# Optimization experiments

Hardware: AMD Instinct MI355X
Metric: run time of the kernel (lower is better)

Reference implementation:

```python
import jax, jax.numpy as jnp
import numpy as np

D_MODEL = 1024
D_STATE = 16
D_CONV = 4
EXPAND = 2
D_INNER = EXPAND * D_MODEL
BATCH = 2
SEQ = 4096


def setup_inputs() -> dict:
    key = jax.random.key(0)
    ks = jax.random.split(key, 8)
    def w(k, shape, fan_in):
        return jax.random.normal(k, shape, jnp.float32) * (fan_in ** -0.5)
    x = jax.random.normal(ks[0], (BATCH, SEQ, D_MODEL), jnp.float32)
    in_proj_w = w(ks[1], (2 * D_INNER, D_MODEL), D_MODEL)
    conv_w = w(ks[2], (D_INNER, 1, D_CONV), D_CONV)          # depthwise conv kernel (OIH, groups=D_INNER)
    conv_b = jnp.zeros((D_INNER,), jnp.float32)
    x_proj_w = w(ks[3], (1 + 2 * D_STATE, D_INNER), D_INNER)
    dt_proj_w = w(ks[4], (D_INNER, 1), D_STATE)               # Linear(1 -> d_inner), see notes
    dt_proj_b = jnp.zeros((D_INNER,), jnp.float32)
    A_log = jnp.log(jnp.tile(jnp.arange(1, D_STATE + 1, dtype=jnp.float32)[None, :], (D_INNER, 1)))
    D = jnp.ones((D_INNER,), jnp.float32)
    out_proj_w = w(ks[5], (D_MODEL, D_INNER), D_INNER)
    return dict(x=x, in_proj_w=in_proj_w, conv_w=conv_w, conv_b=conv_b,
                x_proj_w=x_proj_w, dt_proj_w=dt_proj_w, dt_proj_b=dt_proj_b,
                A_log=A_log, D=D, out_proj_w=out_proj_w)


def _selective_scan(xs, delta, Bm, Cm, A, D):
    # xs, delta: [B, L, d_inner]; Bm, Cm: [B, L, d_state]; A: [d_inner, d_state]
    def step(h, inp):
        x_t, d_t, b_t, c_t = inp                      # [B,di],[B,di],[B,n],[B,n]
        dA = jnp.exp(d_t[..., None] * A)              # [B, di, n]
        h = dA * h + (d_t * x_t)[..., None] * b_t[:, None, :]
        y = jnp.einsum('bdn,bn->bd', h, c_t) + D * x_t
        return h, y
    h0 = jnp.zeros((xs.shape[0], xs.shape[2], A.shape[1]), xs.dtype)
    seq = (jnp.swapaxes(xs, 0, 1), jnp.swapaxes(delta, 0, 1),
           jnp.swapaxes(Bm, 0, 1), jnp.swapaxes(Cm, 0, 1))
    _, ys = jax.lax.scan(step, h0, seq)               # ys: [L, B, di]
    return jnp.swapaxes(ys, 0, 1)


def _mamba(x, in_proj_w, conv_w, conv_b, x_proj_w, dt_proj_w, dt_proj_b, A_log, D, out_proj_w):
    xz = x @ in_proj_w.T                               # [B, L, 2*di]
    xc, z = jnp.split(xz, 2, axis=-1)
    # causal depthwise conv (pad left d_conv-1, truncate to seq_len)
    u = jnp.swapaxes(xc, 1, 2)                         # [B, di, L]
    u = jax.lax.conv_general_dilated(
        u, conv_w, window_strides=(1,), padding=[(D_CONV - 1, 0)],
        feature_group_count=D_INNER, dimension_numbers=('NCH', 'OIH', 'NCH'))
    u = u + conv_b[None, :, None]
    xs = jax.nn.silu(jnp.swapaxes(u, 1, 2))            # [B, L, di]
    dbc = xs @ x_proj_w.T                              # [B, L, 1+2n]
    delta_raw = dbc[..., :1]
    Bm = dbc[..., 1:1 + D_STATE]
    Cm = dbc[..., 1 + D_STATE:]
    delta = jax.nn.softplus(delta_raw @ dt_proj_w.T + dt_proj_b)   # [B, L, di]
    A = -jnp.exp(A_log)
    y = _selective_scan(xs, delta, Bm, Cm, A, D)
    return (y * jax.nn.silu(z)) @ out_proj_w.T


def reference(x, in_proj_w, conv_w, conv_b, x_proj_w, dt_proj_w, dt_proj_b, A_log, D, out_proj_w):
    return _mamba(x, in_proj_w, conv_w, conv_b, x_proj_w, dt_proj_w, dt_proj_b, A_log, D, out_proj_w)
```

## Files before the change

### kernel.cpp

```cpp
#include <hip/hip_runtime.h>
#include <hip/hip_bf16.h>
#include <stdint.h>

typedef __bf16 bf16x8 __attribute__((ext_vector_type(8)));
typedef float  f32x4  __attribute__((ext_vector_type(4)));
typedef unsigned short u16x8 __attribute__((ext_vector_type(8)));

#define TC 64
#define NC 64

__device__ __forceinline__ unsigned short f2bf(float f) {
  unsigned u = __builtin_bit_cast(unsigned, f);
  unsigned r = (u + 0x7fffu + ((u >> 16) & 1u)) >> 16;
  return (unsigned short)r;
}
__device__ __forceinline__ float bf2f(unsigned short s) {
  unsigned u = ((unsigned)s) << 16;
  return __builtin_bit_cast(float, u);
}

__device__ __forceinline__ void gload_lds16(const void* g, void* l) {
  __builtin_amdgcn_global_load_lds(
      (const __attribute__((address_space(1))) unsigned int*)(g),
      (__attribute__((address_space(3))) unsigned int*)(l),
      16, 0, 0);
}

__device__ __forceinline__ void rpowers(float r, float* rp) {
  float r2 = r * r, r4 = r2 * r2, r8 = r4 * r4;
  rp[0] = r;        rp[1] = r2;       rp[2] = r2 * r;   rp[3] = r4;
  rp[4] = r4 * r;   rp[5] = r4 * r2;  rp[6] = rp[5] * r; rp[7] = r8;
  rp[8] = r8 * r;   rp[9] = r8 * r2;  rp[10] = rp[9] * r; rp[11] = r8 * r4;
  rp[12] = rp[11] * r; rp[13] = rp[11] * r2; rp[14] = rp[13] * r; rp[15] = r8 * r8;
}

__global__ __launch_bounds__(256) void cast_bf16_k(const float4* __restrict__ in,
                                                   ushort4* __restrict__ out, int n4) {
  int i = blockIdx.x * 256 + threadIdx.x;
  int stride = gridDim.x * 256;
  for (; i < n4; i += stride) {
    float4 v = in[i];
    ushort4 o;
    o.x = f2bf(v.x); o.y = f2bf(v.y); o.z = f2bf(v.z); o.w = f2bf(v.w);
    out[i] = o;
  }
}

__global__ __launch_bounds__(256) void pad_xw_k(const float* __restrict__ xw,
                                                unsigned short* __restrict__ xwp) {
  int i = blockIdx.x * 256 + threadIdx.x;
  if (i >= 128 * 2048) return;
  int row = i >> 11, col = i & 2047;
  xwp[i] = (row < 33) ? f2bf(xw[row * 2048 + col]) : (unsigned short)0;
}

template <bool BF16OUT>
__global__ __launch_bounds__(256) void gemm_bf16_nt(
    const unsigned short* __restrict__ A, const unsigned short* __restrict__ B,
    void* __restrict__ Cv, int M, int N, int K)
{
  __shared__ __align__(16) unsigned short As[128 * 32];
  __shared__ __align__(16) unsigned short Bs[128 * 32];
  const int tid = threadIdx.x;
  const int m0 = blockIdx.x * 128;
  const int n0 = blockIdx.y * 128;
  const int w = tid >> 6, l = tid & 63;
  const int wr = w >> 1, wc = w & 1;
  const int lr = l & 15, kk = (l >> 4) * 8;

  f32x4 acc[4][4];
#pragma unroll
  for (int mi = 0; mi < 4; ++mi)
#pragma unroll
    for (int ni = 0; ni < 4; ++ni)
      acc[mi][ni] = (f32x4){0.f, 0.f, 0.f, 0.f};

  for (int k0 = 0; k0 < K; k0 += 32) {
#pragma unroll
    for (int i = 0; i < 2; ++i) {
      int q = tid + 256 * i;
      int row = q >> 2, sub = q & 3;
      gload_lds16(A + (size_t)(m0 + row) * K + k0 + sub * 8, &As[q * 8]);
      gload_lds16(B + (size_t)(n0 + row) * K + k0 + sub * 8, &Bs[q * 8]);
    }
    __syncthreads();
    bf16x8 af[4], bfr[4];
#pragma unroll
    for (int mi = 0; mi < 4; ++mi)
      af[mi] = *(const bf16x8*)&As[(wr * 64 + mi * 16 + lr) * 32 + kk];
#pragma unroll
    for (int ni = 0; ni < 4; ++ni)
      bfr[ni] = *(const bf16x8*)&Bs[(wc * 64 + ni * 16 + lr) * 32 + kk];
#pragma unroll
    for (int mi = 0; mi < 4; ++mi)
#pragma unroll
      for (int ni = 0; ni < 4; ++ni)
        acc[mi][ni] = __builtin_amdgcn_mfma_f32_16x16x32_bf16(af[mi], bfr[ni], acc[mi][ni], 0, 0, 0);
    __syncthreads();
  }

#pragma unroll
  for (int mi = 0; mi < 4; ++mi)
#pragma unroll
    for (int ni = 0; ni < 4; ++ni) {
      int gr = m0 + wr * 64 + mi * 16 + (l >> 4) * 4;
      int gc = n0 + wc * 64 + ni * 16 + (l & 15);
#pragma unroll
      for (int j = 0; j < 4; ++j) {
        if (BF16OUT)
          ((unsigned short*)Cv)[(size_t)(gr + j) * N + gc] = f2bf(acc[mi][ni][j]);
        else
          ((float*)Cv)[(size_t)(gr + j) * N + gc] = acc[mi][ni][j];
      }
    }
}

#define CONV_L 16
__global__ __launch_bounds__(256) void conv_silu_k(
    const unsigned short* __restrict__ xzb, const float* __restrict__ cw,
    const float* __restrict__ cb, unsigned short* __restrict__ xsb)
{
  const int b = blockIdx.y;
  const int l0 = blockIdx.x * CONV_L;
  const int d = threadIdx.x * 8;
  float w[4][8], bias[8];
#pragma unroll
  for (int i = 0; i < 8; ++i) {
    bias[i] = cb[d + i];
#pragma unroll
    for (int j = 0; j < 4; ++j) w[j][i] = cw[(d + i) * 4 + j];
  }
  const size_t rb = (size_t)b * 4096;
  float win[3][8];
#pragma unroll
  for (int j = 0; j < 3; ++j) {
    int l = l0 - 3 + j;
    if (l >= 0) {
      u16x8 v = *(const u16x8*)(xzb + (rb + l) * 4096 + d);
#pragma unroll
      for (int i = 0; i < 8; ++i) win[j][i] = bf2f(v[i]);
    } else {
#pragma unroll
      for (int i = 0; i < 8; ++i) win[j][i] = 0.f;
    }
  }
  for (int l = l0; l < l0 + CONV_L; ++l) {
    u16x8 v = *(const u16x8*)(xzb + (rb + l) * 4096 + d);
    float cur[8]; u16x8 ob;
#pragma unroll
    for (int i = 0; i < 8; ++i) {
      cur[i] = bf2f(v[i]);
      float u = bias[i] + w[0][i] * win[0][i] + w[1][i] * win[1][i]
                        + w[2][i] * win[2][i] + w[3][i] * cur[i];
      float s = u / (1.f + __expf(-u));
      ob[i] = f2bf(s);
    }
    *(u16x8*)(xsb + (rb + l) * 2048 + d) = ob;
#pragma unroll
    for (int i = 0; i < 8; ++i) { win[0][i] = win[1][i]; win[1][i] = win[2][i]; win[2][i] = cur[i]; }
  }
}

__global__ __launch_bounds__(256) void scan_p1(
    const unsigned short* __restrict__ xsb16, const float* __restrict__ dbc,
    const float* __restrict__ dtw, const float* __restrict__ dtb,
    const float* __restrict__ alog,
    float* __restrict__ Sg, float* __restrict__ cdg)
{
  const int chunk = blockIdx.x;
  const int d0 = blockIdx.y * 256;
  const int b = blockIdx.z;
  const int tid = threadIdx.x;
  const size_t rowbase = (size_t)b * 4096 + chunk * TC;

  __shared__ __align__(16) unsigned short xsS[TC][256];
  __shared__ __align__(16) float bS[TC][16];
  __shared__ float drS[TC];

  if (tid < TC) drS[tid] = dbc[(rowbase + tid) * 128];
  for (int i = tid; i < TC * 16; i += 256) {
    int t = i >> 4, q = i & 15;
    bS[t][q] = dbc[(rowbase + t) * 128 + 1 + q];
  }
  for (int i = tid; i < TC * 32; i += 256) {
    int t = i >> 5, q = i & 31;
    *(u16x8*)&xsS[t][q * 8] = *(const u16x8*)(xsb16 + (rowbase + t) * 2048 + d0 + q * 8);
  }
  __syncthreads();

  const int d = d0 + tid;
  const float wdt = dtw[d], bdt = dtb[d];
  float adn[16];
  bool ok = true;
#pragma unroll
  for (int k = 0; k < 4; ++k) {
    float4 a4 = *(const float4*)(alog + (size_t)d * 16 + k * 4);
    adn[4 * k + 0] = -__expf(a4.x); adn[4 * k + 1] = -__expf(a4.y);
    adn[4 * k + 2] = -__expf(a4.z); adn[4 * k + 3] = -__expf(a4.w);
  }
#pragma unroll
  for (int n = 0; n < 16; ++n)
    ok = ok && (fabsf(adn[n] + (float)(n + 1)) <= 1e-3f * (float)(n + 1));

  float h[16];
#pragma unroll
  for (int n = 0; n < 16; ++n) h[n] = 0.f;
  float cd = 0.f;

  if (ok) {
    for (int t = 0; t < TC; ++t) {
      float pre = fmaf(drS[t], wdt, bdt);
      float e = __expf(pre);
      float dlt = (pre > 20.f) ? pre : __logf(1.f + e);
      float xv = bf2f(xsS[t][tid]);
      float dx = dlt * xv;
      cd += dlt;
      float r = __expf(-dlt);
      float rp[16];
      rpowers(r, rp);
      f32x4 Bv[4];
#pragma unroll
      for (int k = 0; k < 4; ++k) Bv[k] = ((const f32x4*)&bS[t][0])[k];
#pragma unroll
      for (int n = 0; n < 16; ++n)
        h[n] = fmaf(rp[n], h[n], dx * Bv[n >> 2][n & 3]);
    }
  } else {
    for (int t = 0; t < TC; ++t) {
      float pre = fmaf(drS[t], wdt, bdt);
      float e = __expf(pre);
      float dlt = (pre > 20.f) ? pre : __logf(1.f + e);
      float xv = bf2f(xsS[t][tid]);
      float dx = dlt * xv;
      cd += dlt;
      f32x4 Bv[4];
#pragma unroll
      for (int k = 0; k < 4; ++k) Bv[k] = ((const f32x4*)&bS[t][0])[k];
#pragma unroll
      for (int n = 0; n < 16; ++n) {
        float dA = __expf(adn[n] * dlt);
        h[n] = fmaf(dA, h[n], dx * Bv[n >> 2][n & 3]);
      }
    }
  }
  cdg[(size_t)(b * NC + chunk) * 2048 + d] = cd;
  float* Sp = Sg + ((size_t)(b * NC + chunk) * 32768 + (size_t)d * 16);
#pragma unroll
  for (int k = 0; k < 4; ++k)
    ((float4*)Sp)[k] = make_float4(h[4 * k], h[4 * k + 1], h[4 * k + 2], h[4 * k + 3]);
}

__global__ __launch_bounds__(256) void scan_p2(
    const float* __restrict__ Sg, const float* __restrict__ cdg,
    const float* __restrict__ alog, float* __restrict__ Hg)
{
  int g = blockIdx.x * 256 + threadIdx.x;
  int b = g >> 15, dn = g & 32767;
  int d = dn >> 4;
  float adn = -__expf(alog[dn]);
  float h = 0.f;
  for (int c = 0; c < NC; ++c) {
    size_t o = (size_t)(b * NC + c) * 32768 + dn;
    float P = __expf(adn * cdg[(size_t)(b * NC + c) * 2048 + d]);
    Hg[o] = h;
    h = fmaf(P, h, Sg[o]);
  }
}

__global__ __launch_bounds__(256) void scan_p3(
    const unsigned short* __restrict__ xsb16, const float* __restrict__ dbc,
    const float* __restrict__ dtw, const float* __restrict__ dtb,
    const float* __restrict__ alog, const float* __restrict__ Dp,
    const unsigned short* __restrict__ xzb, const float* __restrict__ Hg,
    unsigned short* __restrict__ gb)
{
  const int chunk = blockIdx.x;
  const int d0 = blockIdx.y * 256;
  const int b = blockIdx.z;
  const int tid = threadIdx.x;
  const size_t rowbase = (size_t)b * 4096 + chunk * TC;

  __shared__ __align__(16) unsigned short xsS[TC][256];
  __shared__ __align__(16) float bcS[TC][32];

  for (int i = tid; i < TC * 32; i += 256) {
    int t = i >> 5, q = i & 31;
    bcS[t][q] = dbc[(rowbase + t) * 128 + 1 + q];
  }
  for (int i = tid; i < TC * 32; i += 256) {
    int t = i >> 5, q = i & 31;
    *(u16x8*)&xsS[t][q * 8] = *(const u16x8*)(xsb16 + (rowbase + t) * 2048 + d0 + q * 8);
  }
  __syncthreads();

  const int d = d0 + tid;
  const float wdt = dtw[d], bdt = dtb[d], Dd = Dp[d];
  const float* __restrict__ drp = dbc + rowbase * 128;
  float adn[16];
  bool ok = true;
#pragma unroll
  for (int k = 0; k < 4; ++k) {
    float4 a4 = *(const float4*)(alog + (size_t)d * 16 + k * 4);
    adn[4 * k + 0] = -__expf(a4.x); adn[4 * k + 1] = -__expf(a4.y);
    adn[4 * k + 2] = -__expf(a4.z); adn[4 * k + 3] = -__expf(a4.w);
  }
#pragma unroll
  for (int n = 0; n < 16; ++n)
    ok = ok && (fabsf(adn[n] + (float)(n + 1)) <= 1e-3f * (float)(n + 1));

  float h[16];
  {
    const float* Hp = Hg + ((size_t)(b * NC + chunk) * 32768 + (size_t)d * 16);
#pragma unroll
    for (int k = 0; k < 4; ++k) {
      float4 h4 = ((const float4*)Hp)[k];
      h[4 * k + 0] = h4.x; h[4 * k + 1] = h4.y; h[4 * k + 2] = h4.z; h[4 * k + 3] = h4.w;
    }
  }

  if (ok) {
    for (int t = 0; t < TC; ++t) {
      float pre = fmaf(drp[(size_t)t * 128], wdt, bdt);
      float e = __expf(pre);
      float dlt = (pre > 20.f) ? pre : __logf(1.f + e);
      float xv = bf2f(xsS[t][tid]);
      float dx = dlt * xv;
      float r = __expf(-dlt);
      float rp[16];
      rpowers(r, rp);
      f32x4 Bv[4], Cv[4];
#pragma unroll
      for (int k = 0; k < 4; ++k) {
        Bv[k] = ((const f32x4*)&bcS[t][0])[k];
        Cv[k] = ((const f32x4*)&bcS[t][16])[k];
      }
      float yp[4];
      yp[0] = Dd * xv; yp[1] = 0.f; yp[2] = 0.f; yp[3] = 0.f;
#pragma unroll
      for (int n = 0; n < 16; ++n) {
        h[n] = fmaf(rp[n], h[n], dx * Bv[n >> 2][n & 3]);
        yp[n & 3] = fmaf(h[n], Cv[n >> 2][n & 3], yp[n & 3]);
      }
      float y = (yp[0] + yp[1]) + (yp[2] + yp[3]);
      xsS[t][tid] = f2bf(y);
    }
  } else {
    for (int t = 0; t < TC; ++t) {
      float pre = fmaf(drp[(size_t)t * 128], wdt, bdt);
      float e = __expf(pre);
      float dlt = (pre > 20.f) ? pre : __logf(1.f + e);
      float xv = bf2f(xsS[t][tid]);
      float dx = dlt * xv;
      f32x4 Bv[4], Cv[4];
#pragma unroll
      for (int k = 0; k < 4; ++k) {
        Bv[k] = ((const f32x4*)&bcS[t][0])[k];
        Cv[k] = ((const f32x4*)&bcS[t][16])[k];
      }
      float yp[4];
      yp[0] = Dd * xv; yp[1] = 0.f; yp[2] = 0.f; yp[3] = 0.f;
#pragma unroll
      for (int n = 0; n < 16; ++n) {
        float dA = __expf(adn[n] * dlt);
        h[n] = fmaf(dA, h[n], dx * Bv[n >> 2][n & 3]);
        yp[n & 3] = fmaf(h[n], Cv[n >> 2][n & 3], yp[n & 3]);
      }
      float y = (yp[0] + yp[1]) + (yp[2] + yp[3]);
      xsS[t][tid] = f2bf(y);
    }
  }
  __syncthreads();

  for (int i = tid; i < TC * 32; i += 256) {
    int t = i >> 5, q = i & 31;
    u16x8 yv = *(const u16x8*)&xsS[t][q * 8];
    u16x8 zv = *(const u16x8*)(xzb + (rowbase + t) * 4096 + 2048 + d0 + q * 8);
    u16x8 ov;
#pragma unroll
    for (int j = 0; j < 8; ++j) {
      float z = bf2f(zv[j]);
      float s = z / (1.f + __expf(-z));
      ov[j] = f2bf(bf2f(yv[j]) * s);
    }
    *(u16x8*)(gb + (rowbase + t) * 2048 + d0 + q * 8) = ov;
  }
}

extern "C" void kernel_launch(void* const* d_in, const int* in_sizes, int n_in,
                              void* d_out, int out_size, void* d_ws, size_t ws_size,
                              hipStream_t stream) {
  const float* x    = (const float*)d_in[0];
  const float* ipw  = (const float*)d_in[1];
  const float* cw   = (const float*)d_in[2];
  const float* cb   = (const float*)d_in[3];
  const float* xpw  = (const float*)d_in[4];
  const float* dtw  = (const float*)d_in[5];
  const float* dtb  = (const float*)d_in[6];
  const float* alog = (const float*)d_in[7];
  const float* Dp   = (const float*)d_in[8];
  const float* opw  = (const float*)d_in[9];
  float* out = (float*)d_out;

  char* p = (char*)d_ws;
  unsigned short* xb   = (unsigned short*)p; p += (size_t)8388608 * 2;
  unsigned short* wb1  = (unsigned short*)p; p += (size_t)4194304 * 2;
  unsigned short* wb2  = (unsigned short*)p; p += (size_t)2097152 * 2;
  unsigned short* xwp  = (unsigned short*)p; p += (size_t)262144 * 2;
  unsigned short* xzb  = (unsigned short*)p; p += (size_t)33554432 * 2;
  unsigned short* xsb16= (unsigned short*)p; p += (size_t)16777216 * 2;
  float*          dbc  = (float*)p;          p += (size_t)1048576 * 4;
  unsigned short* gb   = (unsigned short*)p; p += (size_t)16777216 * 2;
  float*          Sg   = (float*)p;          p += (size_t)4194304 * 4;
  float*          cdg  = (float*)p;          p += (size_t)262144 * 4;
  float*          Hg   = (float*)xb;

  cast_bf16_k<<<1024, 256, 0, stream>>>((const float4*)x,   (ushort4*)xb,  8388608 / 4);
  cast_bf16_k<<<1024, 256, 0, stream>>>((const float4*)ipw, (ushort4*)wb1, 4194304 / 4);
  cast_bf16_k<<<512,  256, 0, stream>>>((const float4*)opw, (ushort4*)wb2, 2097152 / 4);
  pad_xw_k<<<1024, 256, 0, stream>>>(xpw, xwp);

  gemm_bf16_nt<true ><<<dim3(64, 32), 256, 0, stream>>>(xb, wb1, xzb, 8192, 4096, 1024);
  conv_silu_k<<<dim3(4096 / CONV_L, 2), 256, 0, stream>>>(xzb, cw, cb, xsb16);
  gemm_bf16_nt<false><<<dim3(64, 1), 256, 0, stream>>>(xsb16, xwp, dbc, 8192, 128, 2048);

  scan_p1<<<dim3(NC, 8, 2), 256, 0, stream>>>(xsb16, dbc, dtw, dtb, alog, Sg, cdg);
  scan_p2<<<256, 256, 0, stream>>>(Sg, cdg, alog, Hg);
  scan_p3<<<dim3(NC, 8, 2), 256, 0, stream>>>(xsb16, dbc, dtw, dtb, alog, Dp, xzb, Hg, gb);

  gemm_bf16_nt<false><<<dim3(64, 8), 256, 0, stream>>>(gb, wb2, out, 8192, 1024, 2048);
}
```

Before: 341.8 us.

## Split-K the x_proj GEMM and halve scan shared-memory staging

The narrow x_proj GEMM, which launches only 64 blocks, is split along K into four partial GEMMs written to a scratch buffer aliased onto Sg, and a separate kernel sums the partials. This targets the low parallelism of that GEMM, at the cost of an extra kernel launch and the partial-sum traffic. The scan_p1 and scan_p3 kernels now stage xs into shared memory in two 32-step halves instead of one 64-step tile. This cuts shared memory per block to allow more resident blocks, but adds extra barriers.

```diff
diff --git a/kernel.cpp b/kernel.cpp
--- a/kernel.cpp
+++ b/kernel.cpp
@@ -8,6 +8,7 @@
 
 #define TC 64
 #define NC 64
+#define TH 32
 
 __device__ __forceinline__ unsigned short f2bf(float f) {
   unsigned u = __builtin_bit_cast(unsigned, f);
@@ -115,6 +116,76 @@
     }
 }
 
+#define KSPLIT 4
+__global__ __launch_bounds__(256) void gemm_bf16_splitk(
+    const unsigned short* __restrict__ A, const unsigned short* __restrict__ B,
+    float* __restrict__ Cpart, int M, int N, int K)
+{
+  __shared__ __align__(16) unsigned short As[128 * 32];
+  __shared__ __align__(16) unsigned short Bs[128 * 32];
+  const int tid = threadIdx.x;
+  const int m0 = blockIdx.x * 128;
+  const int n0 = 0;
+  const int z = blockIdx.z;
+  const int kseg = K / KSPLIT;
+  const int kbeg = z * kseg;
+  const int w = tid >> 6, l = tid & 63;
+  const int wr = w >> 1, wc = w & 1;
+  const int lr = l & 15, kk = (l >> 4) * 8;
+  float* C = Cpart + (size_t)z * M * N;
+
+  f32x4 acc[4][4];
+#pragma unroll
+  for (int mi = 0; mi < 4; ++mi)
+#pragma unroll
+    for (int ni = 0; ni < 4; ++ni)
+      acc[mi][ni] = (f32x4){0.f, 0.f, 0.f, 0.f};
+
+  for (int k0 = kbeg; k0 < kbeg + kseg; k0 += 32) {
+#pragma unroll
+    for (int i = 0; i < 2; ++i) {
+      int q = tid + 256 * i;
+      int row = q >> 2, sub = q & 3;
+      gload_lds16(A + (size_t)(m0 + row) * K + k0 + sub * 8, &As[q * 8]);
+      gload_lds16(B + (size_t)(n0 + row) * K + k0 + sub * 8, &Bs[q * 8]);
+    }
+    __syncthreads();
+    bf16x8 af[4], bfr[4];
+#pragma unroll
+    for (int mi = 0; mi < 4; ++mi)
+      af[mi] = *(const bf16x8*)&As[(wr * 64 + mi * 16 + lr) * 32 + kk];
+#pragma unroll
+    for (int ni = 0; ni < 4; ++ni)
+      bfr[ni] = *(const bf16x8*)&Bs[(wc * 64 + ni * 16 + lr) * 32 + kk];
+#pragma unroll
+    for (int mi = 0; mi < 4; ++mi)
+#pragma unroll
+      for (int ni = 0; ni < 4; ++ni)
+        acc[mi][ni] = __builtin_amdgcn_mfma_f32_16x16x32_bf16(af[mi], bfr[ni], acc[mi][ni], 0, 0, 0);
+    __syncthreads();
+  }
+
+#pragma unroll
+  for (int mi = 0; mi < 4; ++mi)
+#pragma unroll
+    for (int ni = 0; ni < 4; ++ni) {
+      int gr = m0 + wr * 64 + mi * 16 + (l >> 4) * 4;
+      int gc = n0 + wc * 64 + ni * 16 + (l & 15);
+#pragma unroll
+      for (int j = 0; j < 4; ++j)
+        C[(size_t)(gr + j) * N + gc] = acc[mi][ni][j];
+    }
+}
+
+__global__ __launch_bounds__(256) void redux4_k(const float4* __restrict__ part,
+                                                float4* __restrict__ out) {
+  int i = blockIdx.x * 256 + threadIdx.x;
+  const int STR = 262144;
+  float4 a = part[i], b = part[i + STR], c = part[i + 2 * STR], d = part[i + 3 * STR];
+  out[i] = make_float4(a.x + b.x + c.x + d.x, a.y + b.y + c.y + d.y,
+                       a.z + b.z + c.z + d.z, a.w + b.w + c.w + d.w);
+}
+
 #define CONV_L 16
 __global__ __launch_bounds__(256) void conv_silu_k(
     const unsigned short* __restrict__ xzb, const float* __restrict__ cw,
@@ -173,7 +244,7 @@
   const int tid = threadIdx.x;
   const size_t rowbase = (size_t)b * 4096 + chunk * TC;
 
-  __shared__ __align__(16) unsigned short xsS[TC][256];
+  __shared__ __align__(16) unsigned short xsS[TH][256];
   __shared__ __align__(16) float bS[TC][16];
   __shared__ float drS[TC];
 
@@ -182,11 +253,6 @@
     int t = i >> 4, q = i & 15;
     bS[t][q] = dbc[(rowbase + t) * 128 + 1 + q];
   }
-  for (int i = tid; i < TC * 32; i += 256) {
-    int t = i >> 5, q = i & 31;
-    *(u16x8*)&xsS[t][q * 8] = *(const u16x8*)(xsb16 + (rowbase + t) * 2048 + d0 + q * 8);
-  }
-  __syncthreads();
 
   const int d = d0 + tid;
   const float wdt = dtw[d], bdt = dtb[d];
@@ -207,39 +273,51 @@
   for (int n = 0; n < 16; ++n) h[n] = 0.f;
   float cd = 0.f;
 
-  if (ok) {
-    for (int t = 0; t < TC; ++t) {
-      float pre = fmaf(drS[t], wdt, bdt);
-      float e = __expf(pre);
-      float dlt = (pre > 20.f) ? pre : __logf(1.f + e);
-      float xv = bf2f(xsS[t][tid]);
-      float dx = dlt * xv;
-      cd += dlt;
-      float r = __expf(-dlt);
-      float rp[16];
-      rpowers(r, rp);
-      f32x4 Bv[4];
-#pragma unroll
-      for (int k = 0; k < 4; ++k) Bv[k] = ((const f32x4*)&bS[t][0])[k];
-#pragma unroll
-      for (int n = 0; n < 16; ++n)
-        h[n] = fmaf(rp[n], h[n], dx * Bv[n >> 2][n & 3]);
-    }
-  } else {
-    for (int t = 0; t < TC; ++t) {
-      float pre = fmaf(drS[t], wdt, bdt);
-      float e = __expf(pre);
-      float dlt = (pre > 20.f) ? pre : __logf(1.f + e);
-      float xv = bf2f(xsS[t][tid]);
-      float dx = dlt * xv;
-      cd += dlt;
-      f32x4 Bv[4];
-#pragma unroll
-      for (int k = 0; k < 4; ++k) Bv[k] = ((const f32x4*)&bS[t][0])[k];
-#pragma unroll
-      for (int n = 0; n < 16; ++n) {
-        float dA = __expf(adn[n] * dlt);
-        h[n] = fmaf(dA, h[n], dx * Bv[n >> 2][n & 3]);
+  for (int half = 0; half < 2; ++half) {
+    if (half) __syncthreads();
+    for (int i = tid; i < TH * 32; i += 256) {
+      int tt = i >> 5, q = i & 31;
+      *(u16x8*)&xsS[tt][q * 8] =
+          *(const u16x8*)(xsb16 + (rowbase + half * TH + tt) * 2048 + d0 + q * 8);
+    }
+    __syncthreads();
+
+    if (ok) {
+      for (int tt = 0; tt < TH; ++tt) {
+        int t = half * TH + tt;
+        float pre = fmaf(drS[t], wdt, bdt);
+        float e = __expf(pre);
+        float dlt = (pre > 20.f) ? pre : __logf(1.f + e);
+        float xv = bf2f(xsS[tt][tid]);
+        float dx = dlt * xv;
+        cd += dlt;
+        float r = __expf(-dlt);
+        float rp[16];
+        rpowers(r, rp);
+        f32x4 Bv[4];
+#pragma unroll
+        for (int k = 0; k < 4; ++k) Bv[k] = ((const f32x4*)&bS[t][0])[k];
+#pragma unroll
+        for (int n = 0; n < 16; ++n)
+          h[n] = fmaf(rp[n], h[n], dx * Bv[n >> 2][n & 3]);
+      }
+    } else {
+      for (int tt = 0; tt < TH; ++tt) {
+        int t = half * TH + tt;
+        float pre = fmaf(drS[t], wdt, bdt);
+        float e = __expf(pre);
+        float dlt = (pre > 20.f) ? pre : __logf(1.f + e);
+        float xv = bf2f(xsS[tt][tid]);
+        float dx = dlt * xv;
+        cd += dlt;
+        f32x4 Bv[4];
+#pragma unroll
+        for (int k = 0; k < 4; ++k) Bv[k] = ((const f32x4*)&bS[t][0])[k];
+#pragma unroll
+        for (int n = 0; n < 16; ++n) {
+          float dA = __expf(adn[n] * dlt);
+          h[n] = fmaf(dA, h[n], dx * Bv[n >> 2][n & 3]);
+        }
       }
     }
   }
@@ -280,18 +358,13 @@
   const int tid = threadIdx.x;
   const size_t rowbase = (size_t)b * 4096 + chunk * TC;
 
-  __shared__ __align__(16) unsigned short xsS[TC][256];
+  __shared__ __align__(16) unsigned short xsS[TH][256];
   __shared__ __align__(16) float bcS[TC][32];
 
   for (int i = tid; i < TC * 32; i += 256) {
     int t = i >> 5, q = i & 31;
     bcS[t][q] = dbc[(rowbase + t) * 128 + 1 + q];
   }
-  for (int i = tid; i < TC * 32; i += 256) {
-    int t = i >> 5, q = i & 31;
-    *(u16x8*)&xsS[t][q * 8] = *(const u16x8*)(xsb16 + (rowbase + t) * 2048 + d0 + q * 8);
-  }
-  __syncthreads();
 
   const int d = d0 + tid;
   const float wdt = dtw[d], bdt = dtb[d], Dd = Dp[d];
@@ -318,71 +391,84 @@
     }
   }
 
-  if (ok) {
-    for (int t = 0; t < TC; ++t) {
-      float pre = fmaf(drp[(size_t)t * 128], wdt, bdt);
-      float e = __expf(pre);
-      float dlt = (pre > 20.f) ? pre : __logf(1.f + e);
-      float xv = bf2f(xsS[t][tid]);
-      float dx = dlt * xv;
-      float r = __expf(-dlt);
-      float rp[16];
-      rpowers(r, rp);
-      f32x4 Bv[4], Cv[4];
-#pragma unroll
-      for (int k = 0; k < 4; ++k) {
-        Bv[k] = ((const f32x4*)&bcS[t][0])[k];
-        Cv[k] = ((const f32x4*)&bcS[t][16])[k];
+  for (int half = 0; half < 2; ++half) {
+    if (half) __syncthreads();
+    for (int i = tid; i < TH * 32; i += 256) {
+      int tt = i >> 5, q = i & 31;
+      *(u16x8*)&xsS[tt][q * 8] =
+          *(const u16x8*)(xsb16 + (rowbase + half * TH + tt) * 2048 + d0 + q * 8);
+    }
+    __syncthreads();
+
+    if (ok) {
+      for (int tt = 0; tt < TH; ++tt) {
+        int t = half * TH + tt;
+        float pre = fmaf(drp[(size_t)t * 128], wdt, bdt);
+        float e = __expf(pre);
+        float dlt = (pre > 20.f) ? pre : __logf(1.f + e);
+        float xv = bf2f(xsS[tt][tid]);
+        float dx = dlt * xv;
+        float r = __expf(-dlt);
+        float rp[16];
+        rpowers(r, rp);
+        f32x4 Bv[4], Cv[4];
+#pragma unroll
+        for (int k = 0; k < 4; ++k) {
+          Bv[k] = ((const f32x4*)&bcS[t][0])[k];
+          Cv[k] = ((const f32x4*)&bcS[t][16])[k];
+        }
+        float yp[4];
+        yp[0] = Dd * xv; yp[1] = 0.f; yp[2] = 0.f; yp[3] = 0.f;
+#pragma unroll
+        for (int n = 0; n < 16; ++n) {
+          h[n] = fmaf(rp[n], h[n], dx * Bv[n >> 2][n & 3]);
+          yp[n & 3] = fmaf(h[n], Cv[n >> 2][n & 3], yp[n & 3]);
+        }
+        float y = (yp[0] + yp[1]) + (yp[2] + yp[3]);
+        xsS[tt][tid] = f2bf(y);
       }
-      float yp[4];
-      yp[0] = Dd * xv; yp[1] = 0.f; yp[2] = 0.f; yp[3] = 0.f;
-#pragma unroll
-      for (int n = 0; n < 16; ++n) {
-        h[n] = fmaf(rp[n], h[n], dx * Bv[n >> 2][n & 3]);
-        yp[n & 3] = fmaf(h[n], Cv[n >> 2][n & 3], yp[n & 3]);
+    } else {
+      for (int tt = 0; tt < TH; ++tt) {
+        int t = half * TH + tt;
+        float pre = fmaf(drp[(size_t)t * 128], wdt, bdt);
+        float e = __expf(pre);
+        float dlt = (pre > 20.f) ? pre : __logf(1.f + e);
+        float xv = bf2f(xsS[tt][tid]);
+        float dx = dlt * xv;
+        f32x4 Bv[4], Cv[4];
+#pragma unroll
+        for (int k = 0; k < 4; ++k) {
+          Bv[k] = ((const f32x4*)&bcS[t][0])[k];
+          Cv[k] = ((const f32x4*)&bcS[t][16])[k];
+        }
+        float yp[4];
+        yp[0] = Dd * xv; yp[1] = 0.f; yp[2] = 0.f; yp[3] = 0.f;
+#pragma unroll
+        for (int n = 0; n < 16; ++n) {
+          float dA = __expf(adn[n] * dlt);
+          h[n] = fmaf(dA, h[n], dx * Bv[n >> 2][n & 3]);
+          yp[n & 3] = fmaf(h[n], Cv[n >> 2][n & 3], yp[n & 3]);
+        }
+        float y = (yp[0] + yp[1]) + (yp[2] + yp[3]);
+        xsS[tt][tid] = f2bf(y);
       }
-      float y = (yp[0] + yp[1]) + (yp[2] + yp[3]);
-      xsS[t][tid] = f2bf(y);
-    }
-  } else {
-    for (int t = 0; t < TC; ++t) {
-      float pre = fmaf(drp[(size_t)t * 128], wdt, bdt);
-      float e = __expf(pre);
-      float dlt = (pre > 20.f) ? pre : __logf(1.f + e);
-      float xv = bf2f(xsS[t][tid]);
-      float dx = dlt * xv;
-      f32x4 Bv[4], Cv[4];
-#pragma unroll
-      for (int k = 0; k < 4; ++k) {
-        Bv[k] = ((const f32x4*)&bcS[t][0])[k];
-        Cv[k] = ((const f32x4*)&bcS[t][16])[k];
+    }
+    __syncthreads();
+
+    for (int i = tid; i < TH * 32; i += 256) {
+      int tt = i >> 5, q = i & 31;
+      size_t row = rowbase + half * TH + tt;
+      u16x8 yv = *(const u16x8*)&xsS[tt][q * 8];
+      u16x8 zv = *(const u16x8*)(xzb + row * 4096 + 2048 + d0 + q * 8);
+      u16x8 ov;
+#pragma unroll
+      for (int j = 0; j < 8; ++j) {
+        float z = bf2f(zv[j]);
+        float s = z / (1.f + __expf(-z));
+        ov[j] = f2bf(bf2f(yv[j]) * s);
       }
-      float yp[4];
-      yp[0] = Dd * xv; yp[1] = 0.f; yp[2] = 0.f; yp[3] = 0.f;
-#pragma unroll
-      for (int n = 0; n < 16; ++n) {
-        float dA = __expf(adn[n] * dlt);
-        h[n] = fmaf(dA, h[n], dx * Bv[n >> 2][n & 3]);
-        yp[n & 3] = fmaf(h[n], Cv[n >> 2][n & 3], yp[n & 3]);
-      }
-      float y = (yp[0] + yp[1]) + (yp[2] + yp[3]);
-      xsS[t][tid] = f2bf(y);
-    }
-  }
-  __syncthreads();
-
-  for (int i = tid; i < TC * 32; i += 256) {
-    int t = i >> 5, q = i & 31;
-    u16x8 yv = *(const u16x8*)&xsS[t][q * 8];
-    u16x8 zv = *(const u16x8*)(xzb + (rowbase + t) * 4096 + 2048 + d0 + q * 8);
-    u16x8 ov;
-#pragma unroll
-    for (int j = 0; j < 8; ++j) {
-      float z = bf2f(zv[j]);
-      float s = z / (1.f + __expf(-z));
-      ov[j] = f2bf(bf2f(yv[j]) * s);
-    }
-    *(u16x8*)(gb + (rowbase + t) * 2048 + d0 + q * 8) = ov;
+      *(u16x8*)(gb + row * 2048 + d0 + q * 8) = ov;
+    }
   }
 }
 
@@ -413,6 +499,7 @@
   float*          Sg   = (float*)p;          p += (size_t)4194304 * 4;
   float*          cdg  = (float*)p;          p += (size_t)262144 * 4;
   float*          Hg   = (float*)xb;
+  float*          dbcp = Sg;
 
   cast_bf16_k<<<1024, 256, 0, stream>>>((const float4*)x,   (ushort4*)xb,  8388608 / 4);
   cast_bf16_k<<<1024, 256, 0, stream>>>((const float4*)ipw, (ushort4*)wb1, 4194304 / 4);
@@ -421,7 +508,9 @@
 
   gemm_bf16_nt<true ><<<dim3(64, 32), 256, 0, stream>>>(xb, wb1, xzb, 8192, 4096, 1024);
   conv_silu_k<<<dim3(4096 / CONV_L, 2), 256, 0, stream>>>(xzb, cw, cb, xsb16);
-  gemm_bf16_nt<false><<<dim3(64, 1), 256, 0, stream>>>(xsb16, xwp, dbc, 8192, 128, 2048);
+
+  gemm_bf16_splitk<<<dim3(64, 1, KSPLIT), 256, 0, stream>>>(xsb16, xwp, dbcp, 8192, 128, 2048);
+  redux4_k<<<1024, 256, 0, stream>>>((const float4*)dbcp, (float4*)dbc);
 
   scan_p1<<<dim3(NC, 8, 2), 256, 0, stream>>>(xsb16, dbc, dtw, dtb, alog, Sg, cdg);
   scan_p2<<<256, 256, 0, stream>>>(Sg, cdg, alog, Hg);
```

After: 320.9 us. 1.06x faster.
